# Kernel tuning notes

Hardware: AMD Instinct MI355X
Metric: run time of the kernel (lower is better)

Reference implementation:

```python
import jax, jax.numpy as jnp
import numpy as np

B, R, N = 4, 1024, 100
REG_FG_THRESH = 0.55
EPS = 1e-8


def _cross2(a, b):
    return a[..., 0] * b[..., 1] - a[..., 1] * b[..., 0]


def _corners_bev(box):
    # box: (7,) [x,y,z,dx,dy,dz,heading] -> (4,2) CCW BEV corners
    x, y, dx, dy, ang = box[0], box[1], box[3], box[4], box[6]
    c, s = jnp.cos(ang), jnp.sin(ang)
    lx = jnp.array([0.5, -0.5, -0.5, 0.5], dtype=box.dtype) * dx
    ly = jnp.array([0.5, 0.5, -0.5, -0.5], dtype=box.dtype) * dy
    return jnp.stack([x + lx * c - ly * s, y + lx * s + ly * c], axis=-1)


def _points_in_box(pts, box):
    # pts (P,2), box (7,) -> (P,) bool; transform into box frame
    c, s = jnp.cos(box[6]), jnp.sin(box[6])
    px = pts[:, 0] - box[0]
    py = pts[:, 1] - box[1]
    lx = px * c + py * s
    ly = -px * s + py * c
    return (jnp.abs(lx) <= box[3] * 0.5 + 1e-5) & (jnp.abs(ly) <= box[4] * 0.5 + 1e-5)


def _bev_inter_area(boxa, boxb):
    # exact rotated-rectangle intersection area (convex polygon of <=8 verts)
    ca = _corners_bev(boxa)
    cb = _corners_bev(boxb)
    in_b = _points_in_box(ca, boxb)
    in_a = _points_in_box(cb, boxa)
    a1, a2 = ca, jnp.roll(ca, -1, axis=0)
    b1, b2 = cb, jnp.roll(cb, -1, axis=0)
    d1 = a2 - a1
    d2 = b2 - b1
    denom = _cross2(d1[:, None, :], d2[None, :, :])              # (4,4)
    diff = b1[None, :, :] - a1[:, None, :]                       # (4,4,2)
    safe = jnp.where(jnp.abs(denom) > EPS, denom, EPS)
    t = _cross2(diff, d2[None, :, :]) / safe
    u = _cross2(diff, d1[:, None, :]) / safe
    hit = (jnp.abs(denom) > EPS) & (t >= 0) & (t <= 1) & (u >= 0) & (u <= 1)
    pin = a1[:, None, :] + t[..., None] * d1[:, None, :]         # (4,4,2)
    pts = jnp.concatenate([ca, cb, pin.reshape(16, 2)], axis=0)  # (24,2)
    val = jnp.concatenate([in_b, in_a, hit.reshape(16)], axis=0)
    nv = val.sum()
    ctr = (pts * val[:, None]).sum(0) / jnp.maximum(nv, 1)
    ang = jnp.where(val, jnp.arctan2(pts[:, 1] - ctr[1], pts[:, 0] - ctr[0]), 1e9)
    order = jnp.argsort(ang)
    p = pts[order]
    v = val[order]
    first = p[0]
    p = jnp.where(v[:, None], p, first)   # pad invalid slots with first vertex (zero shoelace contribution)
    q = jnp.roll(p, -1, axis=0)
    area = 0.5 * jnp.abs(jnp.sum(p[:, 0] * q[:, 1] - q[:, 0] * p[:, 1]))
    return jnp.where(nv >= 3, area, jnp.zeros((), dtype=pts.dtype))


def _iou3d_pair(a, b):
    # same math as iou3d_nms_utils.boxes_iou3d_gpu for one pair
    inter_bev = _bev_inter_area(a, b)
    oh = jnp.clip(jnp.minimum(a[2] + a[5] * 0.5, b[2] + b[5] * 0.5)
                  - jnp.maximum(a[2] - a[5] * 0.5, b[2] - b[5] * 0.5), 0.0)
    inter = inter_bev * oh
    va = a[3] * a[4] * a[5]
    vb = b[3] * b[4] * b[5]
    return inter / jnp.clip(va + vb - inter, 1e-6, None)


_iou_rois_gts = jax.vmap(jax.vmap(_iou3d_pair, in_axes=(None, 0)), in_axes=(0, None))  # (R,N)
_iou_batched = jax.vmap(_iou_rois_gts)                                                  # (B,R,N)


def setup_inputs() -> dict:
    key = jax.random.key(0)
    ks = jax.random.split(key, 9)
    xy = jax.random.uniform(ks[0], (B, N, 2), minval=-40.0, maxval=40.0)
    z = jax.random.uniform(ks[1], (B, N, 1), minval=-2.0, maxval=0.0)
    dims = jax.random.uniform(ks[2], (B, N, 3), minval=1.0, maxval=4.5)
    heading = jax.random.uniform(ks[3], (B, N, 1), minval=-np.pi, maxval=np.pi)
    labels = jax.random.randint(ks[4], (B, N, 1), 1, 4).astype(jnp.float32)
    gt_boxes = jnp.concatenate([xy, z, dims, heading, labels], axis=-1)  # (B,N,8)
    # sampling ROIs are jittered GT boxes, mirroring generate_sampling_roi
    base_idx = jax.random.randint(ks[5], (B, R), 0, N)
    base = jnp.take_along_axis(gt_boxes[..., :7], base_idx[..., None], axis=1)  # (B,R,7)
    ctr_off = jax.random.uniform(ks[6], (B, R, 3), minval=-0.5, maxval=0.5) * base[..., 3:6]
    scale = jax.random.uniform(ks[7], (B, R, 3), minval=0.8, maxval=1.25)
    ang_off = jax.random.uniform(ks[8], (B, R, 1), minval=-np.pi / 4, maxval=np.pi / 4)
    sampling_rois = jnp.concatenate(
        [base[..., :3] + ctr_off, base[..., 3:6] * scale, base[..., 6:7] + ang_off], axis=-1)
    sampling_rois_labels = jnp.take_along_axis(gt_boxes[..., 7], base_idx, axis=1).astype(jnp.int32)
    return {"sampling_rois": sampling_rois,
            "sampling_rois_labels": sampling_rois_labels,
            "gt_boxes": gt_boxes}


def reference(sampling_rois, sampling_rois_labels, gt_boxes):
    # sample_rois_for_rcnn core: all-pairs rotated 3D IoU, best-GT assignment,
    # gather gt_of_rois, then forward()'s reg_valid_mask thresholding.
    iou3d = _iou_batched(sampling_rois, gt_boxes[..., :7])        # (B,R,N)
    max_overlaps = iou3d.max(axis=-1)                             # (B,R)
    gt_assignment = iou3d.argmax(axis=-1)                         # (B,R)
    gt_of_rois = jnp.take_along_axis(gt_boxes, gt_assignment[..., None], axis=1)  # (B,R,8)
    reg_valid_mask = (max_overlaps > REG_FG_THRESH).astype(jnp.int32)
    return sampling_rois, gt_of_rois, max_overlaps, sampling_rois_labels, reg_valid_mask
```

## Files before the change

kernel.cpp:

```cpp
#include <hip/hip_runtime.h>
#include <math.h>

#define BB 4
#define RR 1024
#define NN 100
#define NROI (BB * RR)
#define RPB 4
#define PPB (RPB * NN)
#define NBLK (NROI / RPB)

#define INIT_PACK 0x00000000FFFFFFFFull

__device__ __forceinline__ void corner_of(int i, float cx0, float cy0, float dx, float dy,
                                          float c, float s, float& X, float& Y) {
    float sx = (i == 0 || i == 3) ? 0.5f : -0.5f;
    float sy = (i <= 1) ? 0.5f : -0.5f;
    float lx = sx * dx, ly = sy * dy;
    X = cx0 + lx * c - ly * s;
    Y = cy0 + lx * s + ly * c;
}

__global__ __launch_bounds__(256) void sampling_target_fused(
    const float* __restrict__ rois,
    const int*   __restrict__ labels,
    const float* __restrict__ gts,
    float*       __restrict__ out)
{
    __shared__ float s_gts[NN * 9];
    __shared__ float s_rois[RPB * 7];
    __shared__ int   s_list[PPB];
    __shared__ int   s_cnt;
    __shared__ unsigned long long s_best[RPB];

    const int tid = threadIdx.x;
    const int roi0 = blockIdx.x * RPB;
    const int b = roi0 >> 10;

    for (int i = tid; i < NN * 8; i += 256)
        s_gts[(i >> 3) * 9 + (i & 7)] = gts[b * NN * 8 + i];
    if (tid < RPB * 7) s_rois[tid] = rois[roi0 * 7 + tid];
    if (tid < RPB) s_best[tid] = INIT_PACK;
    if (tid == 0) s_cnt = 0;
    __syncthreads();

    for (int p = tid; p < PPB; p += 256) {
        int rl = p / NN;
        int n = p - rl * NN;
        const float* A = &s_rois[rl * 7];
        const float* G = &s_gts[n * 9];
        float oh = fminf(A[2] + A[5] * 0.5f, G[2] + G[5] * 0.5f)
                 - fmaxf(A[2] - A[5] * 0.5f, G[2] - G[5] * 0.5f);
        float dxc = A[0] - G[0], dyc = A[1] - G[1];
        float ra = 0.5f * sqrtf(A[3] * A[3] + A[4] * A[4]);
        float rb = 0.5f * sqrtf(G[3] * G[3] + G[4] * G[4]);
        float rr = ra + rb;
        if (oh > 0.0f && dxc * dxc + dyc * dyc <= rr * rr) {
            int pos = atomicAdd(&s_cnt, 1);
            s_list[pos] = p;
        }
    }
    __syncthreads();

    const int cnt = s_cnt;
    const int g = tid >> 5;
    const int lane = tid & 31;
    const int half = (tid >> 5) & 1;

    for (int i = g; i < cnt; i += 8) {
        int p = s_list[i];
        int rl = p / NN;
        int n = p - rl * NN;
        const float* A = &s_rois[rl * 7];
        const float* G = &s_gts[n * 9];
        float ax = A[0], ay = A[1], az = A[2], adx = A[3], ady = A[4], adz = A[5], aang = A[6];
        float gx_ = G[0], gy_ = G[1], gz_ = G[2], gdx = G[3], gdy = G[4], gdz = G[5], gang = G[6];
        float acs = cosf(aang), asn = sinf(aang);
        float bcs = cosf(gang), bsn = sinf(gang);

        float ppx = 0.0f, ppy = 0.0f;
        bool val = false;
        if (lane < 4) {
            corner_of(lane, ax, ay, adx, ady, acs, asn, ppx, ppy);
            float qx = ppx - gx_, qy = ppy - gy_;
            float lx = qx * bcs + qy * bsn;
            float ly = -qx * bsn + qy * bcs;
            val = (fabsf(lx) <= gdx * 0.5f + 1e-5f) && (fabsf(ly) <= gdy * 0.5f + 1e-5f);
        } else if (lane < 8) {
            corner_of(lane - 4, gx_, gy_, gdx, gdy, bcs, bsn, ppx, ppy);
            float qx = ppx - ax, qy = ppy - ay;
            float lx = qx * acs + qy * asn;
            float ly = -qx * asn + qy * acs;
            val = (fabsf(lx) <= adx * 0.5f + 1e-5f) && (fabsf(ly) <= ady * 0.5f + 1e-5f);
        } else if (lane < 24) {
            int e = lane - 8;
            int ii = e >> 2, jj = e & 3;
            float a1x, a1y, a2x, a2y, b1x, b1y, b2x, b2y;
            corner_of(ii, ax, ay, adx, ady, acs, asn, a1x, a1y);
            corner_of((ii + 1) & 3, ax, ay, adx, ady, acs, asn, a2x, a2y);
            corner_of(jj, gx_, gy_, gdx, gdy, bcs, bsn, b1x, b1y);
            corner_of((jj + 1) & 3, gx_, gy_, gdx, gdy, bcs, bsn, b2x, b2y);
            float d1x = a2x - a1x, d1y = a2y - a1y;
            float d2x = b2x - b1x, d2y = b2y - b1y;
            float denom = d1x * d2y - d1y * d2x;
            float fx = b1x - a1x, fy = b1y - a1y;
            float safe = (fabsf(denom) > 1e-8f) ? denom : 1e-8f;
            float t = (fx * d2y - fy * d2x) / safe;
            float u = (fx * d1y - fy * d1x) / safe;
            ppx = a1x + t * d1x;
            ppy = a1y + t * d1y;
            val = (fabsf(denom) > 1e-8f) && (t >= 0.0f) && (t <= 1.0f) && (u >= 0.0f) && (u <= 1.0f);
        }

        unsigned long long m = __ballot(val);
        unsigned gm = (unsigned)(half ? (m >> 32) : (m & 0xFFFFFFFFull));
        int nv = __popc(gm);

        float inter_bev = 0.0f;
        if (nv >= 3) {
            float sx = val ? ppx : 0.0f;
            float sy = val ? ppy : 0.0f;
#pragma unroll
            for (int off = 16; off; off >>= 1) {
                sx += __shfl_xor(sx, off, 32);
                sy += __shfl_xor(sy, off, 32);
            }
            float cx = sx / (float)nv, cy = sy / (float)nv;

            float myAng = val ? atan2f(ppy - cy, ppx - cx) : 1e9f;

            float sAng = 1e30f; int sIdx = 0; bool found = false;
            float gAng = 1e30f; int gIdx = 0;
#pragma unroll
            for (int j = 0; j < 24; j++) {
                float aj = __shfl(myAng, j, 32);
                if (aj < 1e8f) {
                    bool greater = (aj > myAng) || (aj == myAng && j > lane);
                    if (greater && aj < sAng) { sAng = aj; sIdx = j; found = true; }
                    if (aj < gAng) { gAng = aj; gIdx = j; }
                }
            }
            int qi = found ? sIdx : gIdx;
            float qx = __shfl(ppx, qi, 32);
            float qy = __shfl(ppy, qi, 32);
            float contrib = val ? (ppx * qy - qx * ppy) : 0.0f;
#pragma unroll
            for (int off = 16; off; off >>= 1)
                contrib += __shfl_xor(contrib, off, 32);
            inter_bev = 0.5f * fabsf(contrib);
        }

        if (lane == 0) {
            float oh = fminf(az + adz * 0.5f, gz_ + gdz * 0.5f)
                     - fmaxf(az - adz * 0.5f, gz_ - gdz * 0.5f);
            float inter = inter_bev * oh;
            float va = adx * ady * adz;
            float vb = gdx * gdy * gdz;
            float v = inter / fmaxf(va + vb - inter, 1e-6f);
            unsigned long long packed =
                ((unsigned long long)__float_as_uint(v) << 32) | (unsigned)(~(unsigned)n);
            atomicMax(&s_best[rl], packed);
        }
    }
    __syncthreads();

    if (tid < RPB) {
        int r = roi0 + tid;
        unsigned long long packed = s_best[tid];
        float mo = __uint_as_float((unsigned)(packed >> 32));
        int besti = (int)(~(unsigned)(packed & 0xFFFFFFFFu));

        float* out_rois = out;
        float* out_gor  = out + NROI * 7;
        float* out_max  = out_gor + NROI * 8;
        float* out_lab  = out_max + NROI;
        float* out_msk  = out_lab + NROI;

#pragma unroll
        for (int k = 0; k < 7; k++) out_rois[r * 7 + k] = s_rois[tid * 7 + k];
#pragma unroll
        for (int k = 0; k < 8; k++) out_gor[r * 8 + k] = s_gts[besti * 9 + k];
        out_max[r] = mo;
        out_lab[r] = (float)labels[r];
        out_msk[r] = (mo > 0.55f) ? 1.0f : 0.0f;
    }
}

extern "C" void kernel_launch(void* const* d_in, const int* in_sizes, int n_in,
                              void* d_out, int out_size, void* d_ws, size_t ws_size,
                              hipStream_t stream) {
    const float* rois   = (const float*)d_in[0];
    const int*   labels = (const int*)d_in[1];
    const float* gts    = (const float*)d_in[2];
    float* out = (float*)d_out;

    hipLaunchKernelGGL(sampling_target_fused, dim3(NBLK), dim3(256), 0, stream,
                       rois, labels, gts, out);
}
```

Before: 67.42 us.

## Assign one wavefront per ROI with ballot-based candidate lists, no shared memory

Restructures the kernel so each 64-lane wavefront owns a single ROI. The wavefront builds its candidate GT list with ballots in registers instead of a shared-memory atomic list, and processes two candidate pairs at a time, one per 32-lane half. Shared-memory staging, block-wide barriers and shared atomics are removed, and the best IoU is reduced in registers with a single cross-half shuffle. The cost is that GT boxes are read straight from global or cache memory for each pair, and the work per wavefront is less balanced because each ROI has a different number of candidates.

```diff
diff --git a/kernel.cpp b/kernel.cpp
--- a/kernel.cpp
+++ b/kernel.cpp
@@ -5,9 +5,6 @@
 #define RR 1024
 #define NN 100
 #define NROI (BB * RR)
-#define RPB 4
-#define PPB (RPB * NN)
-#define NBLK (NROI / RPB)
 
 #define INIT_PACK 0x00000000FFFFFFFFull
 
@@ -20,85 +17,87 @@
     Y = cy0 + lx * s + ly * c;
 }
 
-__global__ __launch_bounds__(256) void sampling_target_fused(
+__global__ __launch_bounds__(256) void sampling_target_wave(
     const float* __restrict__ rois,
     const int*   __restrict__ labels,
     const float* __restrict__ gts,
     float*       __restrict__ out)
 {
-    __shared__ float s_gts[NN * 9];
-    __shared__ float s_rois[RPB * 7];
-    __shared__ int   s_list[PPB];
-    __shared__ int   s_cnt;
-    __shared__ unsigned long long s_best[RPB];
-
-    const int tid = threadIdx.x;
-    const int roi0 = blockIdx.x * RPB;
-    const int b = roi0 >> 10;
-
-    for (int i = tid; i < NN * 8; i += 256)
-        s_gts[(i >> 3) * 9 + (i & 7)] = gts[b * NN * 8 + i];
-    if (tid < RPB * 7) s_rois[tid] = rois[roi0 * 7 + tid];
-    if (tid < RPB) s_best[tid] = INIT_PACK;
-    if (tid == 0) s_cnt = 0;
-    __syncthreads();
-
-    for (int p = tid; p < PPB; p += 256) {
-        int rl = p / NN;
-        int n = p - rl * NN;
-        const float* A = &s_rois[rl * 7];
-        const float* G = &s_gts[n * 9];
-        float oh = fminf(A[2] + A[5] * 0.5f, G[2] + G[5] * 0.5f)
-                 - fmaxf(A[2] - A[5] * 0.5f, G[2] - G[5] * 0.5f);
-        float dxc = A[0] - G[0], dyc = A[1] - G[1];
-        float ra = 0.5f * sqrtf(A[3] * A[3] + A[4] * A[4]);
-        float rb = 0.5f * sqrtf(G[3] * G[3] + G[4] * G[4]);
-        float rr = ra + rb;
-        if (oh > 0.0f && dxc * dxc + dyc * dyc <= rr * rr) {
-            int pos = atomicAdd(&s_cnt, 1);
-            s_list[pos] = p;
-        }
-    }
-    __syncthreads();
-
-    const int cnt = s_cnt;
-    const int g = tid >> 5;
-    const int lane = tid & 31;
-    const int half = (tid >> 5) & 1;
-
-    for (int i = g; i < cnt; i += 8) {
-        int p = s_list[i];
-        int rl = p / NN;
-        int n = p - rl * NN;
-        const float* A = &s_rois[rl * 7];
-        const float* G = &s_gts[n * 9];
-        float ax = A[0], ay = A[1], az = A[2], adx = A[3], ady = A[4], adz = A[5], aang = A[6];
-        float gx_ = G[0], gy_ = G[1], gz_ = G[2], gdx = G[3], gdy = G[4], gdz = G[5], gang = G[6];
-        float acs = cosf(aang), asn = sinf(aang);
+    const int r    = (int)((blockIdx.x * blockDim.x + threadIdx.x) >> 6);
+    const int lane = threadIdx.x & 63;
+    if (r >= NROI) return;
+    const int b = r >> 10;
+    const float* gbase = gts + b * NN * 8;
+
+    const float* A = rois + r * 7;
+    const float ax = A[0], ay = A[1], az = A[2];
+    const float adx = A[3], ady = A[4], adz = A[5], aang = A[6];
+    const float ra   = 0.5f * sqrtf(adx * adx + ady * ady);
+    const float azlo = az - adz * 0.5f, azhi = az + adz * 0.5f;
+
+    unsigned long long m0, m1;
+    {
+        unsigned long long mm[2];
+#pragma unroll
+        for (int it = 0; it < 2; it++) {
+            int n = it * 64 + lane;
+            bool pass = false;
+            if (n < NN) {
+                const float* G = gbase + n * 8;
+                float gx = G[0], gy = G[1], gz = G[2];
+                float gdx = G[3], gdy = G[4], gdz = G[5];
+                float oh = fminf(azhi, gz + gdz * 0.5f) - fmaxf(azlo, gz - gdz * 0.5f);
+                float dxc = ax - gx, dyc = ay - gy;
+                float rb = 0.5f * sqrtf(gdx * gdx + gdy * gdy);
+                float rr = ra + rb;
+                pass = (oh > 0.0f) && (dxc * dxc + dyc * dyc <= rr * rr);
+            }
+            mm[it] = __ballot(pass);
+        }
+        m0 = mm[0]; m1 = mm[1];
+    }
+
+    const float acs = cosf(aang), asn = sinf(aang);
+    const int half = lane >> 5;
+    const int l32  = lane & 31;
+
+    unsigned long long best = INIT_PACK;
+
+    while (m0 | m1) {
+        int na, nb = -1;
+        if (m0) { na = __ffsll((unsigned long long)m0) - 1;      m0 &= m0 - 1; }
+        else    { na = __ffsll((unsigned long long)m1) - 1 + 64; m1 &= m1 - 1; }
+        if (m0)      { nb = __ffsll((unsigned long long)m0) - 1;      m0 &= m0 - 1; }
+        else if (m1) { nb = __ffsll((unsigned long long)m1) - 1 + 64; m1 &= m1 - 1; }
+
+        const int  myN    = half ? nb : na;
+        const bool active = (myN >= 0);
+        const float* G = gbase + (active ? myN : 0) * 8;
+        float gx = G[0], gy = G[1], gz = G[2];
+        float gdx = G[3], gdy = G[4], gdz = G[5], gang = G[6];
         float bcs = cosf(gang), bsn = sinf(gang);
 
         float ppx = 0.0f, ppy = 0.0f;
         bool val = false;
-        if (lane < 4) {
-            corner_of(lane, ax, ay, adx, ady, acs, asn, ppx, ppy);
-            float qx = ppx - gx_, qy = ppy - gy_;
+        if (l32 < 4) {
+            corner_of(l32, ax, ay, adx, ady, acs, asn, ppx, ppy);
+            float qx = ppx - gx, qy = ppy - gy;
             float lx = qx * bcs + qy * bsn;
             float ly = -qx * bsn + qy * bcs;
             val = (fabsf(lx) <= gdx * 0.5f + 1e-5f) && (fabsf(ly) <= gdy * 0.5f + 1e-5f);
-        } else if (lane < 8) {
-            corner_of(lane - 4, gx_, gy_, gdx, gdy, bcs, bsn, ppx, ppy);
+        } else if (l32 < 8) {
+            corner_of(l32 - 4, gx, gy, gdx, gdy, bcs, bsn, ppx, ppy);
             float qx = ppx - ax, qy = ppy - ay;
             float lx = qx * acs + qy * asn;
             float ly = -qx * asn + qy * acs;
             val = (fabsf(lx) <= adx * 0.5f + 1e-5f) && (fabsf(ly) <= ady * 0.5f + 1e-5f);
-        } else if (lane < 24) {
-            int e = lane - 8;
-            int ii = e >> 2, jj = e & 3;
+        } else if (l32 < 24) {
+            int e = l32 - 8, ii = e >> 2, jj = e & 3;
             float a1x, a1y, a2x, a2y, b1x, b1y, b2x, b2y;
             corner_of(ii, ax, ay, adx, ady, acs, asn, a1x, a1y);
             corner_of((ii + 1) & 3, ax, ay, adx, ady, acs, asn, a2x, a2y);
-            corner_of(jj, gx_, gy_, gdx, gdy, bcs, bsn, b1x, b1y);
-            corner_of((jj + 1) & 3, gx_, gy_, gdx, gdy, bcs, bsn, b2x, b2y);
+            corner_of(jj, gx, gy, gdx, gdy, bcs, bsn, b1x, b1y);
+            corner_of((jj + 1) & 3, gx, gy, gdx, gdy, bcs, bsn, b2x, b2y);
             float d1x = a2x - a1x, d1y = a2y - a1y;
             float d2x = b2x - b1x, d2y = b2y - b1y;
             float denom = d1x * d2y - d1y * d2x;
@@ -110,9 +109,10 @@
             ppy = a1y + t * d1y;
             val = (fabsf(denom) > 1e-8f) && (t >= 0.0f) && (t <= 1.0f) && (u >= 0.0f) && (u <= 1.0f);
         }
-
-        unsigned long long m = __ballot(val);
-        unsigned gm = (unsigned)(half ? (m >> 32) : (m & 0xFFFFFFFFull));
+        val = val && active;
+
+        unsigned long long bm = __ballot(val);
+        unsigned gm = half ? (unsigned)(bm >> 32) : (unsigned)(bm & 0xFFFFFFFFull);
         int nv = __popc(gm);
 
         float inter_bev = 0.0f;
@@ -134,7 +134,7 @@
             for (int j = 0; j < 24; j++) {
                 float aj = __shfl(myAng, j, 32);
                 if (aj < 1e8f) {
-                    bool greater = (aj > myAng) || (aj == myAng && j > lane);
+                    bool greater = (aj > myAng) || (aj == myAng && j > l32);
                     if (greater && aj < sAng) { sAng = aj; sIdx = j; found = true; }
                     if (aj < gAng) { gAng = aj; gIdx = j; }
                 }
@@ -149,38 +149,42 @@
             inter_bev = 0.5f * fabsf(contrib);
         }
 
-        if (lane == 0) {
-            float oh = fminf(az + adz * 0.5f, gz_ + gdz * 0.5f)
-                     - fmaxf(az - adz * 0.5f, gz_ - gdz * 0.5f);
+        if (active) {
+            float oh = fminf(azhi, gz + gdz * 0.5f) - fmaxf(azlo, gz - gdz * 0.5f);
             float inter = inter_bev * oh;
             float va = adx * ady * adz;
             float vb = gdx * gdy * gdz;
             float v = inter / fmaxf(va + vb - inter, 1e-6f);
             unsigned long long packed =
-                ((unsigned long long)__float_as_uint(v) << 32) | (unsigned)(~(unsigned)n);
-            atomicMax(&s_best[rl], packed);
-        }
-    }
-    __syncthreads();
-
-    if (tid < RPB) {
-        int r = roi0 + tid;
-        unsigned long long packed = s_best[tid];
-        float mo = __uint_as_float((unsigned)(packed >> 32));
-        int besti = (int)(~(unsigned)(packed & 0xFFFFFFFFu));
-
-        float* out_rois = out;
-        float* out_gor  = out + NROI * 7;
-        float* out_max  = out_gor + NROI * 8;
-        float* out_lab  = out_max + NROI;
-        float* out_msk  = out_lab + NROI;
-
-#pragma unroll
-        for (int k = 0; k < 7; k++) out_rois[r * 7 + k] = s_rois[tid * 7 + k];
-#pragma unroll
-        for (int k = 0; k < 8; k++) out_gor[r * 8 + k] = s_gts[besti * 9 + k];
+                ((unsigned long long)__float_as_uint(v) << 32) | (unsigned)(~(unsigned)myN);
+            best = (packed > best) ? packed : best;
+        }
+    }
+
+    {
+        unsigned long long other = __shfl(best, lane ^ 32, 64);
+        best = (other > best) ? other : best;
+    }
+
+    float mo = __uint_as_float((unsigned)(best >> 32));
+    int besti = (int)(~(unsigned)(best & 0xFFFFFFFFu));
+
+    float* out_rois = out;
+    float* out_gor  = out + NROI * 7;
+    float* out_max  = out_gor + NROI * 8;
+    float* out_lab  = out_max + NROI;
+    float* out_msk  = out_lab + NROI;
+
+    if (lane < 7) {
+        out_rois[r * 7 + lane] = A[lane];
+    } else if (lane < 15) {
+        int k = lane - 7;
+        out_gor[r * 8 + k] = gbase[besti * 8 + k];
+    } else if (lane == 15) {
         out_max[r] = mo;
+    } else if (lane == 16) {
         out_lab[r] = (float)labels[r];
+    } else if (lane == 17) {
         out_msk[r] = (mo > 0.55f) ? 1.0f : 0.0f;
     }
 }
@@ -193,6 +197,6 @@
     const float* gts    = (const float*)d_in[2];
     float* out = (float*)d_out;
 
-    hipLaunchKernelGGL(sampling_target_fused, dim3(NBLK), dim3(256), 0, stream,
+    hipLaunchKernelGGL(sampling_target_wave, dim3(NROI / 4), dim3(256), 0, stream,
                        rois, labels, gts, out);
 }
```

Result: slower. 72.71 us (+7.8%).

## Precompute per-box trig, corners and extents in shared memory; halve ROIs per block

Applied to the files above, without the earlier changes.

Each block now precomputes cos/sin, corner coordinates, z-extents, radii and volumes once per GT box and ROI, storing them in structure-of-arrays shared memory. Without this, every wavefront pair recomputes trig and corners for each candidate pair. RPB drops from 4 to 2, which doubles the block count to spread work across more CUs, and the output writes are spread across threads with float4 GT loads. The cost is that each block repeats the GT precompute (100 sincos), and there are twice as many blocks doing it.

```diff
diff --git a/kernel.cpp b/kernel.cpp
--- a/kernel.cpp
+++ b/kernel.cpp
@@ -5,7 +5,7 @@
 #define RR 1024
 #define NN 100
 #define NROI (BB * RR)
-#define RPB 4
+#define RPB 2
 #define PPB (RPB * NN)
 #define NBLK (NROI / RPB)
 
@@ -26,8 +26,12 @@
     const float* __restrict__ gts,
     float*       __restrict__ out)
 {
-    __shared__ float s_gts[NN * 9];
-    __shared__ float s_rois[RPB * 7];
+    __shared__ float s_gx[NN], s_gy[NN], s_gzlo[NN], s_gzhi[NN], s_grb[NN];
+    __shared__ float s_bcs[NN], s_bsn[NN], s_bhx[NN], s_bhy[NN], s_vb[NN];
+    __shared__ float s_gcx[4][NN], s_gcy[4][NN];
+    __shared__ float s_ax[RPB], s_ay[RPB], s_azlo[RPB], s_azhi[RPB], s_ara[RPB];
+    __shared__ float s_acs[RPB], s_asn[RPB], s_ahx[RPB], s_ahy[RPB], s_va[RPB];
+    __shared__ float s_acx[RPB][4], s_acy[RPB][4];
     __shared__ int   s_list[PPB];
     __shared__ int   s_cnt;
     __shared__ unsigned long long s_best[RPB];
@@ -36,27 +40,62 @@
     const int roi0 = blockIdx.x * RPB;
     const int b = roi0 >> 10;
 
-    for (int i = tid; i < NN * 8; i += 256)
-        s_gts[(i >> 3) * 9 + (i & 7)] = gts[b * NN * 8 + i];
-    if (tid < RPB * 7) s_rois[tid] = rois[roi0 * 7 + tid];
-    if (tid < RPB) s_best[tid] = INIT_PACK;
-    if (tid == 0) s_cnt = 0;
+    if (tid < NN) {
+        const float4* gp = (const float4*)(gts + (b * NN + tid) * 8);
+        float4 g0 = gp[0];
+        float4 g1 = gp[1];
+        float gx = g0.x, gy = g0.y, gz = g0.z, gdx = g0.w;
+        float gdy = g1.x, gdz = g1.y, gang = g1.z;
+        s_gx[tid] = gx; s_gy[tid] = gy;
+        s_gzlo[tid] = gz - gdz * 0.5f;
+        s_gzhi[tid] = gz + gdz * 0.5f;
+        s_grb[tid] = 0.5f * sqrtf(gdx * gdx + gdy * gdy);
+        float c = cosf(gang), s = sinf(gang);
+        s_bcs[tid] = c; s_bsn[tid] = s;
+        s_bhx[tid] = gdx * 0.5f + 1e-5f;
+        s_bhy[tid] = gdy * 0.5f + 1e-5f;
+        s_vb[tid] = gdx * gdy * gdz;
+#pragma unroll
+        for (int i = 0; i < 4; i++) {
+            float X, Y;
+            corner_of(i, gx, gy, gdx, gdy, c, s, X, Y);
+            s_gcx[i][tid] = X; s_gcy[i][tid] = Y;
+        }
+    } else if (tid < NN + RPB) {
+        int rl = tid - NN;
+        const float* A = rois + (roi0 + rl) * 7;
+        float ax = A[0], ay = A[1], az = A[2];
+        float adx = A[3], ady = A[4], adz = A[5], aang = A[6];
+        s_ax[rl] = ax; s_ay[rl] = ay;
+        s_azlo[rl] = az - adz * 0.5f;
+        s_azhi[rl] = az + adz * 0.5f;
+        s_ara[rl] = 0.5f * sqrtf(adx * adx + ady * ady);
+        float c = cosf(aang), s = sinf(aang);
+        s_acs[rl] = c; s_asn[rl] = s;
+        s_ahx[rl] = adx * 0.5f + 1e-5f;
+        s_ahy[rl] = ady * 0.5f + 1e-5f;
+        s_va[rl] = adx * ady * adz;
+#pragma unroll
+        for (int i = 0; i < 4; i++) {
+            float X, Y;
+            corner_of(i, ax, ay, adx, ady, c, s, X, Y);
+            s_acx[rl][i] = X; s_acy[rl][i] = Y;
+        }
+        s_best[rl] = INIT_PACK;
+    } else if (tid == NN + RPB) {
+        s_cnt = 0;
+    }
     __syncthreads();
 
-    for (int p = tid; p < PPB; p += 256) {
-        int rl = p / NN;
-        int n = p - rl * NN;
-        const float* A = &s_rois[rl * 7];
-        const float* G = &s_gts[n * 9];
-        float oh = fminf(A[2] + A[5] * 0.5f, G[2] + G[5] * 0.5f)
-                 - fmaxf(A[2] - A[5] * 0.5f, G[2] - G[5] * 0.5f);
-        float dxc = A[0] - G[0], dyc = A[1] - G[1];
-        float ra = 0.5f * sqrtf(A[3] * A[3] + A[4] * A[4]);
-        float rb = 0.5f * sqrtf(G[3] * G[3] + G[4] * G[4]);
-        float rr = ra + rb;
+    if (tid < PPB) {
+        int rl = tid / NN;
+        int n = tid - rl * NN;
+        float oh = fminf(s_azhi[rl], s_gzhi[n]) - fmaxf(s_azlo[rl], s_gzlo[n]);
+        float dxc = s_ax[rl] - s_gx[n], dyc = s_ay[rl] - s_gy[n];
+        float rr = s_ara[rl] + s_grb[n];
         if (oh > 0.0f && dxc * dxc + dyc * dyc <= rr * rr) {
             int pos = atomicAdd(&s_cnt, 1);
-            s_list[pos] = p;
+            s_list[pos] = tid;
         }
     }
     __syncthreads();
@@ -70,35 +109,32 @@
         int p = s_list[i];
         int rl = p / NN;
         int n = p - rl * NN;
-        const float* A = &s_rois[rl * 7];
-        const float* G = &s_gts[n * 9];
-        float ax = A[0], ay = A[1], az = A[2], adx = A[3], ady = A[4], adz = A[5], aang = A[6];
-        float gx_ = G[0], gy_ = G[1], gz_ = G[2], gdx = G[3], gdy = G[4], gdz = G[5], gang = G[6];
-        float acs = cosf(aang), asn = sinf(aang);
-        float bcs = cosf(gang), bsn = sinf(gang);
+        float ax = s_ax[rl], ay = s_ay[rl], acs = s_acs[rl], asn = s_asn[rl];
+        float ahx = s_ahx[rl], ahy = s_ahy[rl];
+        float gx = s_gx[n], gy = s_gy[n], bcs = s_bcs[n], bsn = s_bsn[n];
+        float bhx = s_bhx[n], bhy = s_bhy[n];
 
         float ppx = 0.0f, ppy = 0.0f;
         bool val = false;
         if (lane < 4) {
-            corner_of(lane, ax, ay, adx, ady, acs, asn, ppx, ppy);
-            float qx = ppx - gx_, qy = ppy - gy_;
+            ppx = s_acx[rl][lane]; ppy = s_acy[rl][lane];
+            float qx = ppx - gx, qy = ppy - gy;
             float lx = qx * bcs + qy * bsn;
             float ly = -qx * bsn + qy * bcs;
-            val = (fabsf(lx) <= gdx * 0.5f + 1e-5f) && (fabsf(ly) <= gdy * 0.5f + 1e-5f);
+            val = (fabsf(lx) <= bhx) && (fabsf(ly) <= bhy);
         } else if (lane < 8) {
-            corner_of(lane - 4, gx_, gy_, gdx, gdy, bcs, bsn, ppx, ppy);
+            int i4 = lane - 4;
+            ppx = s_gcx[i4][n]; ppy = s_gcy[i4][n];
             float qx = ppx - ax, qy = ppy - ay;
             float lx = qx * acs + qy * asn;
             float ly = -qx * asn + qy * acs;
-            val = (fabsf(lx) <= adx * 0.5f + 1e-5f) && (fabsf(ly) <= ady * 0.5f + 1e-5f);
+            val = (fabsf(lx) <= ahx) && (fabsf(ly) <= ahy);
         } else if (lane < 24) {
-            int e = lane - 8;
-            int ii = e >> 2, jj = e & 3;
-            float a1x, a1y, a2x, a2y, b1x, b1y, b2x, b2y;
-            corner_of(ii, ax, ay, adx, ady, acs, asn, a1x, a1y);
-            corner_of((ii + 1) & 3, ax, ay, adx, ady, acs, asn, a2x, a2y);
-            corner_of(jj, gx_, gy_, gdx, gdy, bcs, bsn, b1x, b1y);
-            corner_of((jj + 1) & 3, gx_, gy_, gdx, gdy, bcs, bsn, b2x, b2y);
+            int e = lane - 8, ii = e >> 2, jj = e & 3;
+            float a1x = s_acx[rl][ii],        a1y = s_acy[rl][ii];
+            float a2x = s_acx[rl][(ii+1)&3],  a2y = s_acy[rl][(ii+1)&3];
+            float b1x = s_gcx[jj][n],         b1y = s_gcy[jj][n];
+            float b2x = s_gcx[(jj+1)&3][n],   b2y = s_gcy[(jj+1)&3][n];
             float d1x = a2x - a1x, d1y = a2y - a1y;
             float d2x = b2x - b1x, d2y = b2y - b1y;
             float denom = d1x * d2y - d1y * d2x;
@@ -111,8 +147,8 @@
             val = (fabsf(denom) > 1e-8f) && (t >= 0.0f) && (t <= 1.0f) && (u >= 0.0f) && (u <= 1.0f);
         }
 
-        unsigned long long m = __ballot(val);
-        unsigned gm = (unsigned)(half ? (m >> 32) : (m & 0xFFFFFFFFull));
+        unsigned long long bm = __ballot(val);
+        unsigned gm = half ? (unsigned)(bm >> 32) : (unsigned)(bm & 0xFFFFFFFFull);
         int nv = __popc(gm);
 
         float inter_bev = 0.0f;
@@ -150,12 +186,9 @@
         }
 
         if (lane == 0) {
-            float oh = fminf(az + adz * 0.5f, gz_ + gdz * 0.5f)
-                     - fmaxf(az - adz * 0.5f, gz_ - gdz * 0.5f);
+            float oh = fminf(s_azhi[rl], s_gzhi[n]) - fmaxf(s_azlo[rl], s_gzlo[n]);
             float inter = inter_bev * oh;
-            float va = adx * ady * adz;
-            float vb = gdx * gdy * gdz;
-            float v = inter / fmaxf(va + vb - inter, 1e-6f);
+            float v = inter / fmaxf(s_va[rl] + s_vb[n] - inter, 1e-6f);
             unsigned long long packed =
                 ((unsigned long long)__float_as_uint(v) << 32) | (unsigned)(~(unsigned)n);
             atomicMax(&s_best[rl], packed);
@@ -163,25 +196,28 @@
     }
     __syncthreads();
 
-    if (tid < RPB) {
-        int r = roi0 + tid;
-        unsigned long long packed = s_best[tid];
-        float mo = __uint_as_float((unsigned)(packed >> 32));
-        int besti = (int)(~(unsigned)(packed & 0xFFFFFFFFu));
-
-        float* out_rois = out;
-        float* out_gor  = out + NROI * 7;
-        float* out_max  = out_gor + NROI * 8;
-        float* out_lab  = out_max + NROI;
-        float* out_msk  = out_lab + NROI;
-
-#pragma unroll
-        for (int k = 0; k < 7; k++) out_rois[r * 7 + k] = s_rois[tid * 7 + k];
-#pragma unroll
-        for (int k = 0; k < 8; k++) out_gor[r * 8 + k] = s_gts[besti * 9 + k];
-        out_max[r] = mo;
-        out_lab[r] = (float)labels[r];
-        out_msk[r] = (mo > 0.55f) ? 1.0f : 0.0f;
+    float* out_rois = out;
+    float* out_gor  = out + NROI * 7;
+    float* out_max  = out_gor + NROI * 8;
+    float* out_lab  = out_max + NROI;
+    float* out_msk  = out_lab + NROI;
+
+    if (tid < RPB * 7) {
+        out_rois[roi0 * 7 + tid] = rois[roi0 * 7 + tid];
+    } else if (tid >= 16 && tid < 16 + RPB * 8) {
+        int k = tid - 16, rl = k >> 3, kk = k & 7;
+        int besti = (int)(~(unsigned)(s_best[rl] & 0xFFFFFFFFu));
+        out_gor[(roi0 + rl) * 8 + kk] = gts[(b * NN + besti) * 8 + kk];
+    } else if (tid >= 32 && tid < 32 + RPB) {
+        int rl = tid - 32;
+        out_max[roi0 + rl] = __uint_as_float((unsigned)(s_best[rl] >> 32));
+    } else if (tid >= 40 && tid < 40 + RPB) {
+        int rl = tid - 40;
+        out_lab[roi0 + rl] = (float)labels[roi0 + rl];
+    } else if (tid >= 48 && tid < 48 + RPB) {
+        int rl = tid - 48;
+        float mo = __uint_as_float((unsigned)(s_best[rl] >> 32));
+        out_msk[roi0 + rl] = (mo > 0.55f) ? 1.0f : 0.0f;
     }
 }
 
```

After: 68.11 us. No clear change (+1.0%).
